# Optimization experiments

Hardware: AMD Instinct MI355X
Metric: run time of the kernel (lower is better)

The kernel has to match this reference:

```python
import jax, jax.numpy as jnp
import numpy as np

N = 8192          # num nodes
E = 262144        # num edges (avg degree 32)
D_IN = 512        # input feature dim
LAT = 128         # latent_dim


def gcn_conv(x, W, b, row, col, n):
    """PyG GCNConv: gcn_norm adds self-loops (weight 1), symmetric normalization,
    message = norm * (x @ W)[row], aggregated at col, plus bias."""
    sl = jnp.arange(n)
    r = jnp.concatenate([row, sl])
    c = jnp.concatenate([col, sl])
    deg = jax.ops.segment_sum(jnp.ones(r.shape[0], dtype=x.dtype), c, num_segments=n)
    dis = jnp.where(deg > 0, deg ** -0.5, 0.0).astype(x.dtype)
    norm = dis[r] * dis[c]                      # [E']
    h = x @ W                                   # [n, out]
    out = jax.ops.segment_sum(h[r] * norm[:, None], c, num_segments=n)
    return out + b


def setup_inputs() -> dict:
    key = jax.random.key(0)
    ks = jax.random.split(key, 12)
    x = jax.random.normal(ks[0], (N, D_IN), dtype=jnp.float32)
    edge_index = jax.random.randint(ks[1], (2, E), 0, N, dtype=jnp.int64)
    h1 = 2 * LAT
    W1 = jax.random.normal(ks[2], (D_IN, h1), dtype=jnp.float32) * (1.0 / np.sqrt(D_IN))
    b1 = jnp.zeros((h1,), dtype=jnp.float32)
    W2 = jax.random.normal(ks[3], (h1, LAT), dtype=jnp.float32) * (1.0 / np.sqrt(h1))
    b2 = jnp.zeros((LAT,), dtype=jnp.float32)
    Wmu = jax.random.normal(ks[4], (LAT, LAT), dtype=jnp.float32) * (1.0 / np.sqrt(LAT))
    bmu = jnp.zeros((LAT,), dtype=jnp.float32)
    Wlv = jax.random.normal(ks[5], (LAT, LAT), dtype=jnp.float32) * (1.0 / np.sqrt(LAT))
    blv = jnp.zeros((LAT,), dtype=jnp.float32)
    return {"x": x, "edge_index": edge_index, "W1": W1, "b1": b1, "W2": W2,
            "b2": b2, "Wmu": Wmu, "bmu": bmu, "Wlv": Wlv, "blv": blv}


def reference(x, edge_index, W1, b1, W2, b2, Wmu, bmu, Wlv, blv):
    n = x.shape[0]
    # GraphVAE.forward: add_self_loops(edge_index) once (GCNConv's gcn_norm adds them again)
    sl = jnp.arange(n)
    row = jnp.concatenate([edge_index[0], sl])
    col = jnp.concatenate([edge_index[1], sl])
    z = jax.nn.relu(gcn_conv(x, W1, b1, row, col, n))
    z = gcn_conv(z, W2, b2, row, col, n)
    mu = z @ Wmu + bmu
    logvar = z @ Wlv + blv
    # eval-mode reparameterize: z = mu (deterministic)
    adj = jax.nn.sigmoid(mu @ mu.T)   # [N, N]
    return adj, mu, logvar
```

## Files before the change

### kernel.cpp

```cpp
#include <hip/hip_runtime.h>
#include <hip/hip_bf16.h>

#define NNODES 8192
#define DIN 512
#define HD1 256
#define LATD 128
#define CAP 128

typedef __attribute__((ext_vector_type(4))) float f32x4;
typedef __attribute__((ext_vector_type(8))) short short8;

__device__ __forceinline__ float bf2f(uint u){
  union { uint i; float f; } v; v.i = u << 16; return v.f;
}
__device__ __forceinline__ ushort f2bf(float f){
  union { float f; uint i; } v; v.f = f;
  uint i = v.i;
  i += 0x7FFFu + ((i >> 16) & 1u);
  return (ushort)(i >> 16);
}


__global__ __launch_bounds__(256) void k_init(const float* __restrict__ W1,
    const float* __restrict__ W2, const float* __restrict__ Wmu,
    const float* __restrict__ Wlv, int* __restrict__ cnt,
    ushort* __restrict__ W1b, ushort* __restrict__ W2b, ushort* __restrict__ Wcb)
{
  const int stride = gridDim.x * 256;
  const int i = blockIdx.x * 256 + threadIdx.x;
  if (i < NNODES) cnt[i] = 0;
  for (int j = i; j < DIN * HD1; j += stride) W1b[j] = f2bf(W1[j]);
  for (int j = i; j < HD1 * LATD; j += stride) W2b[j] = f2bf(W2[j]);
  for (int j = i; j < LATD * 2 * LATD; j += stride){
    const int k = j >> 8, n = j & 255;
    Wcb[j] = f2bf(n < LATD ? Wmu[k * LATD + n] : Wlv[k * LATD + n - LATD]);
  }
}


__global__ __launch_bounds__(256) void k_fill_gemm1(const int* __restrict__ erow,
    const int* __restrict__ ecol, int E, int nbF,
    int* __restrict__ cursor, int* __restrict__ csr,
    const float* __restrict__ x, const ushort* __restrict__ W1b, ushort* __restrict__ h1)
{
  if ((int)blockIdx.x < nbF){
    int e = blockIdx.x * 256 + threadIdx.x;
    if (e < E){
      int r = erow[e], c = ecol[e];
      int pos = atomicAdd(&cursor[c], 1);
      if (pos < CAP) csr[(size_t)c * CAP + pos] = r;
    }
    return;
  }
  const int bx = blockIdx.x - nbF;
  const int n0 = (bx & 3) * 64, m0 = (bx >> 2) * 64;
  __shared__ ushort Al[64][40];
  __shared__ ushort Bl[64][40];
  const int t = threadIdx.x, w = t >> 6, l = t & 63, lr = l & 15, lk = l >> 4;
  const int wm = (w >> 1) * 32, wn = (w & 1) * 32;
  f32x4 acc[2][2] = {};
  for (int kt = 0; kt < DIN / 32; ++kt){
    {
      const int row = t >> 2, ch = t & 3;
      const float* ap = x + (size_t)(m0 + row) * DIN + kt * 32 + ch * 8;
      float4 v0 = *(const float4*)ap;
      float4 v1 = *(const float4*)(ap + 4);
      ushort* d = &Al[row][ch * 8];
      d[0] = f2bf(v0.x); d[1] = f2bf(v0.y); d[2] = f2bf(v0.z); d[3] = f2bf(v0.w);
      d[4] = f2bf(v1.x); d[5] = f2bf(v1.y); d[6] = f2bf(v1.z); d[7] = f2bf(v1.w);
      const int kk = t >> 3, nn = (t & 7) * 8;
      short8 bv = *(const short8*)(W1b + (size_t)(kt * 32 + kk) * HD1 + n0 + nn);
      #pragma unroll
      for (int i = 0; i < 8; ++i) Bl[nn + i][kk] = ((ushort*)&bv)[i];
    }
    __syncthreads();
    short8 a0 = *(const short8*)(&Al[wm + lr][lk * 8]);
    short8 a1 = *(const short8*)(&Al[wm + 16 + lr][lk * 8]);
    short8 b0 = *(const short8*)(&Bl[wn + lr][lk * 8]);
    short8 b1 = *(const short8*)(&Bl[wn + 16 + lr][lk * 8]);
    acc[0][0] = __builtin_amdgcn_mfma_f32_16x16x32_bf16(a0, b0, acc[0][0], 0, 0, 0);
    acc[0][1] = __builtin_amdgcn_mfma_f32_16x16x32_bf16(a0, b1, acc[0][1], 0, 0, 0);
    acc[1][0] = __builtin_amdgcn_mfma_f32_16x16x32_bf16(a1, b0, acc[1][0], 0, 0, 0);
    acc[1][1] = __builtin_amdgcn_mfma_f32_16x16x32_bf16(a1, b1, acc[1][1], 0, 0, 0);
    __syncthreads();
  }
  #pragma unroll
  for (int mi = 0; mi < 2; ++mi){
    #pragma unroll
    for (int ni = 0; ni < 2; ++ni){
      const int row = m0 + wm + mi * 16 + lk * 4;
      const int col = n0 + wn + ni * 16 + lr;
      #pragma unroll
      for (int r = 0; r < 4; ++r)
        h1[(size_t)(row + r) * HD1 + col] = f2bf(acc[mi][ni][r]);
    }
  }
}


__global__ __launch_bounds__(256) void gemm2_kernel(const ushort* __restrict__ A,
    const ushort* __restrict__ Bb, ushort* __restrict__ Cb)
{
  __shared__ ushort Al[32][40];
  __shared__ ushort Bl[64][40];
  const int t = threadIdx.x, w = t >> 6, l = t & 63, lr = l & 15, lk = l >> 4;
  const int m0 = blockIdx.y * 32, n0 = blockIdx.x * 64;
  const int wm = (w >> 1) * 16, wn = (w & 1) * 32;
  f32x4 acc[2] = {};
  for (int kt = 0; kt < HD1 / 32; ++kt){
    {
      const int row = t >> 3, ch = (t & 7) * 4;
      *(uint2*)(&Al[row][ch]) = *(const uint2*)(A + (size_t)(m0 + row) * HD1 + kt * 32 + ch);
      const int kk = t >> 3, nn = (t & 7) * 8;
      short8 bv = *(const short8*)(Bb + (size_t)(kt * 32 + kk) * LATD + n0 + nn);
      #pragma unroll
      for (int i = 0; i < 8; ++i) Bl[nn + i][kk] = ((ushort*)&bv)[i];
    }
    __syncthreads();
    short8 a = *(const short8*)(&Al[wm + lr][lk * 8]);
    short8 b0 = *(const short8*)(&Bl[wn + lr][lk * 8]);
    short8 b1 = *(const short8*)(&Bl[wn + 16 + lr][lk * 8]);
    acc[0] = __builtin_amdgcn_mfma_f32_16x16x32_bf16(a, b0, acc[0], 0, 0, 0);
    acc[1] = __builtin_amdgcn_mfma_f32_16x16x32_bf16(a, b1, acc[1], 0, 0, 0);
    __syncthreads();
  }
  #pragma unroll
  for (int ni = 0; ni < 2; ++ni){
    const int row = m0 + wm + lk * 4;
    const int col = n0 + wn + ni * 16 + lr;
    #pragma unroll
    for (int r = 0; r < 4; ++r)
      Cb[(size_t)(row + r) * LATD + col] = f2bf(acc[ni][r]);
  }
}


__global__ __launch_bounds__(256) void gemm_mulv(const ushort* __restrict__ A,
    const ushort* __restrict__ Bb, const float* __restrict__ bmu,
    const float* __restrict__ blv, float* __restrict__ mu,
    ushort* __restrict__ mu_bf, float* __restrict__ lv)
{
  __shared__ ushort Al[64][40];
  __shared__ ushort Bl[64][40];
  const int t = threadIdx.x, w = t >> 6, l = t & 63, lr = l & 15, lk = l >> 4;
  const int n0 = blockIdx.x * 64, m0 = blockIdx.y * 64;
  const bool is_mu = n0 < LATD;
  const int wm = (w >> 1) * 32, wn = (w & 1) * 32;
  f32x4 acc[2][2] = {};
  for (int kt = 0; kt < LATD / 32; ++kt){
    {
      const int row = t >> 2, ch = t & 3;
      *(short8*)(&Al[row][ch * 8]) =
        *(const short8*)(A + (size_t)(m0 + row) * LATD + kt * 32 + ch * 8);
      const int kk = t >> 3, nn = (t & 7) * 8;
      short8 bv = *(const short8*)(Bb + (size_t)(kt * 32 + kk) * (2 * LATD) + n0 + nn);
      #pragma unroll
      for (int i = 0; i < 8; ++i) Bl[nn + i][kk] = ((ushort*)&bv)[i];
    }
    __syncthreads();
    short8 a0 = *(const short8*)(&Al[wm + lr][lk * 8]);
    short8 a1 = *(const short8*)(&Al[wm + 16 + lr][lk * 8]);
    short8 b0 = *(const short8*)(&Bl[wn + lr][lk * 8]);
    short8 b1 = *(const short8*)(&Bl[wn + 16 + lr][lk * 8]);
    acc[0][0] = __builtin_amdgcn_mfma_f32_16x16x32_bf16(a0, b0, acc[0][0], 0, 0, 0);
    acc[0][1] = __builtin_amdgcn_mfma_f32_16x16x32_bf16(a0, b1, acc[0][1], 0, 0, 0);
    acc[1][0] = __builtin_amdgcn_mfma_f32_16x16x32_bf16(a1, b0, acc[1][0], 0, 0, 0);
    acc[1][1] = __builtin_amdgcn_mfma_f32_16x16x32_bf16(a1, b1, acc[1][1], 0, 0, 0);
    __syncthreads();
  }
  #pragma unroll
  for (int mi = 0; mi < 2; ++mi){
    #pragma unroll
    for (int ni = 0; ni < 2; ++ni){
      const int row = m0 + wm + mi * 16 + lk * 4;
      const int col = n0 + wn + ni * 16 + lr;
      const float bb = is_mu ? bmu[col] : blv[col - LATD];
      #pragma unroll
      for (int r = 0; r < 4; ++r){
        const float v = acc[mi][ni][r] + bb;
        if (is_mu){
          mu[(size_t)(row + r) * LATD + col] = v;
          mu_bf[(size_t)(row + r) * LATD + col] = f2bf(v);
        } else {
          lv[(size_t)(row + r) * LATD + col - LATD] = v;
        }
      }
    }
  }
}


template<int F, bool RELU>
__global__ __launch_bounds__(256) void agg_kernel(const ushort* __restrict__ h,
    const float* __restrict__ bias, const int* __restrict__ cnt,
    const int* __restrict__ csr, ushort* __restrict__ out)
{
  constexpr int LPE = F / 8;
  constexpr int EPI = 64 / LPE;
  __shared__ int2 meta[4][64];
  const int w = threadIdx.x >> 6, l = threadIdx.x & 63;
  const int v = blockIdx.x * 4 + w;
  const int deg = min(cnt[v], CAP);
  const float dv = rsqrtf((float)(deg + 2));
  const int sub = l / LPE;
  const int eb = (l % LPE) * 8;
  float acc[8] = {0.f, 0.f, 0.f, 0.f, 0.f, 0.f, 0.f, 0.f};

  const int beg = v * CAP, end = beg + deg;
  for (int base = beg; base < end; base += 64){
    const int cc = min(64, end - base);
    int idx = 0; float nr = 0.f;
    if (base + l < end){
      idx = csr[base + l];
      nr = rsqrtf((float)(min(cnt[idx], CAP) + 2)) * dv;
    }
    int2 m; m.x = idx; m.y = __float_as_int(nr);
    meta[w][l] = m;
    asm volatile("s_waitcnt lgkmcnt(0)" ::: "memory");
    const int nIt = (cc + EPI - 1) / EPI;
    for (int it = 0; it < nIt; ++it){
      int2 mm = meta[w][it * EPI + sub];
      const float nrr = __int_as_float(mm.y);
      const uint4 r = *(const uint4*)(h + (size_t)mm.x * F + eb);
      acc[0] += nrr * bf2f(r.x & 0xffff); acc[1] += nrr * bf2f(r.x >> 16);
      acc[2] += nrr * bf2f(r.y & 0xffff); acc[3] += nrr * bf2f(r.y >> 16);
      acc[4] += nrr * bf2f(r.z & 0xffff); acc[5] += nrr * bf2f(r.z >> 16);
      acc[6] += nrr * bf2f(r.w & 0xffff); acc[7] += nrr * bf2f(r.w >> 16);
    }
    asm volatile("s_waitcnt lgkmcnt(0)" ::: "memory");
  }
  #pragma unroll
  for (int off = LPE; off < 64; off <<= 1){
    #pragma unroll
    for (int j = 0; j < 8; ++j) acc[j] += __shfl_xor(acc[j], off);
  }
  if (l < LPE){
    const float ss = 2.f * dv * dv;
    const uint4 r = *(const uint4*)(h + (size_t)v * F + eb);
    acc[0] += ss * bf2f(r.x & 0xffff); acc[1] += ss * bf2f(r.x >> 16);
    acc[2] += ss * bf2f(r.y & 0xffff); acc[3] += ss * bf2f(r.y >> 16);
    acc[4] += ss * bf2f(r.z & 0xffff); acc[5] += ss * bf2f(r.z >> 16);
    acc[6] += ss * bf2f(r.w & 0xffff); acc[7] += ss * bf2f(r.w >> 16);
    float4 b0 = *(const float4*)(bias + eb);
    float4 b1 = *(const float4*)(bias + eb + 4);
    acc[0] += b0.x; acc[1] += b0.y; acc[2] += b0.z; acc[3] += b0.w;
    acc[4] += b1.x; acc[5] += b1.y; acc[6] += b1.z; acc[7] += b1.w;
    if (RELU){
      #pragma unroll
      for (int j = 0; j < 8; ++j) acc[j] = fmaxf(acc[j], 0.f);
    }
    uint4 o;
    o.x = (uint)f2bf(acc[0]) | ((uint)f2bf(acc[1]) << 16);
    o.y = (uint)f2bf(acc[2]) | ((uint)f2bf(acc[3]) << 16);
    o.z = (uint)f2bf(acc[4]) | ((uint)f2bf(acc[5]) << 16);
    o.w = (uint)f2bf(acc[6]) | ((uint)f2bf(acc[7]) << 16);
    *(uint4*)(out + (size_t)v * F + eb) = o;
  }
}


__global__ __launch_bounds__(512) void gemm5_kernel(const ushort* __restrict__ mu,
                                                    float* __restrict__ adj)
{
  __shared__ char lds[65536];
  const int t = threadIdx.x;
  const int bj = blockIdx.x, bi = blockIdx.y;
  {
    const int row = t >> 2, ch = t & 3;
    const char* srcA = (const char*)(mu + (size_t)(bi * 128 + row) * LATD);
    const char* srcB = (const char*)(mu + (size_t)(bj * 128 + row) * LATD);
    char* dA = lds + row * 256;
    char* dB = lds + 32768 + row * 256;
    #pragma unroll
    for (int i = 0; i < 4; ++i){
      const int kb = ch * 64 + i * 16;
      const int sk = kb ^ ((row & 7) << 4);
      *(short8*)(dA + sk) = *(const short8*)(srcA + kb);
      *(short8*)(dB + sk) = *(const short8*)(srcB + kb);
    }
  }
  __syncthreads();
  const int wid = t >> 6, l = t & 63, lr = l & 15, lk = l >> 4;
  const int wm = (wid >> 2) * 64, wn = (wid & 3) * 32;
  f32x4 acc[4][2] = {};
  #pragma unroll
  for (int ks = 0; ks < 4; ++ks){
    short8 a[4], b[2];
    const int kb = ks * 64 + lk * 16;
    #pragma unroll
    for (int mi = 0; mi < 4; ++mi){
      const int r = wm + mi * 16 + lr;
      a[mi] = *(const short8*)(lds + r * 256 + (kb ^ ((r & 7) << 4)));
    }
    #pragma unroll
    for (int ni = 0; ni < 2; ++ni){
      const int r = wn + ni * 16 + lr;
      b[ni] = *(const short8*)(lds + 32768 + r * 256 + (kb ^ ((r & 7) << 4)));
    }
    #pragma unroll
    for (int mi = 0; mi < 4; ++mi)
      #pragma unroll
      for (int ni = 0; ni < 2; ++ni)
        acc[mi][ni] = __builtin_amdgcn_mfma_f32_16x16x32_bf16(a[mi], b[ni], acc[mi][ni], 0, 0, 0);
  }
  float* orow = adj + (size_t)(bi * 128 + wm + lk * 4) * NNODES + bj * 128 + wn + lr;
  #pragma unroll
  for (int mi = 0; mi < 4; ++mi){
    #pragma unroll
    for (int ni = 0; ni < 2; ++ni){
      #pragma unroll
      for (int r = 0; r < 4; ++r){
        const float x = acc[mi][ni][r];
        orow[(size_t)(mi * 16 + r) * NNODES + ni * 16] = 1.f / (1.f + __expf(-x));
      }
    }
  }
}


extern "C" void kernel_launch(void* const* d_in, const int* in_sizes, int n_in,
                              void* d_out, int out_size, void* d_ws, size_t ws_size,
                              hipStream_t stream)
{
  const float* x    = (const float*)d_in[0];
  const int*   ei   = (const int*)d_in[1];
  const float* W1   = (const float*)d_in[2];
  const float* b1   = (const float*)d_in[3];
  const float* W2   = (const float*)d_in[4];
  const float* b2   = (const float*)d_in[5];
  const float* Wmu  = (const float*)d_in[6];
  const float* bmu  = (const float*)d_in[7];
  const float* Wlv  = (const float*)d_in[8];
  const float* blv  = (const float*)d_in[9];
  const int E = in_sizes[1] / 2;
  const int* erow = ei;
  const int* ecol = ei + E;

  char* ws = (char*)d_ws;
  int*    cnt   = (int*)(ws);
  ushort* W1b   = (ushort*)(ws + 65536);
  ushort* W2b   = (ushort*)(ws + 327680);
  ushort* Wcb   = (ushort*)(ws + 393216);
  int*    csr   = (int*)(ws + 1048576);
  ushort* h1    = (ushort*)(ws + 8388608);
  ushort* z1    = (ushort*)(ws + 12582912);
  ushort* h2    = (ushort*)(ws + 16777216);
  ushort* z2    = (ushort*)(ws + 18874368);
  ushort* mu_bf = (ushort*)(ws + 20971520);

  float* adj = (float*)d_out;
  float* mu  = adj + (size_t)NNODES * NNODES;
  float* lv  = mu + (size_t)NNODES * LATD;

  const int nbF = (E + 255) / 256;

  k_init<<<128, 256, 0, stream>>>(W1, W2, Wmu, Wlv, cnt, W1b, W2b, Wcb);
  k_fill_gemm1<<<nbF + 4 * (NNODES / 64), 256, 0, stream>>>(
      erow, ecol, E, nbF, cnt, csr, x, W1b, h1);
  agg_kernel<HD1, true><<<NNODES / 4, 256, 0, stream>>>(h1, b1, cnt, csr, z1);
  gemm2_kernel<<<dim3(LATD / 64, NNODES / 32), 256, 0, stream>>>(z1, W2b, h2);
  agg_kernel<LATD, false><<<NNODES / 4, 256, 0, stream>>>(h2, b2, cnt, csr, z2);
  gemm_mulv<<<dim3(2 * LATD / 64, NNODES / 64), 256, 0, stream>>>(
      z2, Wcb, bmu, blv, mu, mu_bf, lv);
  gemm5_kernel<<<dim3(NNODES / 128, NNODES / 128), 512, 0, stream>>>(mu_bf, adj);
}
```

Before: 129.2 us.

## Reorder second GCN layer as aggregate-then-GEMM and fuse with mu/logvar GEMM

The second GCN layer now aggregates z1 (width 256) first and then multiplies by W2, using linearity (A·(z1·W2) = (A·z1)·W2). The W2 GEMM and the mu/logvar GEMM are fused into one kernel that keeps z2 in LDS. GEMM1 and the fused kernel load operands straight from global memory into registers, using weights pre-transposed to a K-contiguous layout, so the LDS staging and barriers are gone. The cost is a second aggregation pass at width 256 instead of 128, which doubles that gather traffic, plus a one-time strided weight transpose.

Result: slower. 168.3 us (+30.3%).

```diff
diff --git a/kernel.cpp b/kernel.cpp
--- a/kernel.cpp
+++ b/kernel.cpp
@@ -19,21 +19,49 @@
   i += 0x7FFFu + ((i >> 16) & 1u);
   return (ushort)(i >> 16);
 }
+__device__ __forceinline__ short8 pack8(float4 v0, float4 v1){
+  short8 s;
+  s[0] = (short)f2bf(v0.x); s[1] = (short)f2bf(v0.y);
+  s[2] = (short)f2bf(v0.z); s[3] = (short)f2bf(v0.w);
+  s[4] = (short)f2bf(v1.x); s[5] = (short)f2bf(v1.y);
+  s[6] = (short)f2bf(v1.z); s[7] = (short)f2bf(v1.w);
+  return s;
+}
 
 
 __global__ __launch_bounds__(256) void k_init(const float* __restrict__ W1,
     const float* __restrict__ W2, const float* __restrict__ Wmu,
     const float* __restrict__ Wlv, int* __restrict__ cnt,
-    ushort* __restrict__ W1b, ushort* __restrict__ W2b, ushort* __restrict__ Wcb)
+    ushort* __restrict__ W1t, ushort* __restrict__ W2t, ushort* __restrict__ Wct)
 {
   const int stride = gridDim.x * 256;
-  const int i = blockIdx.x * 256 + threadIdx.x;
-  if (i < NNODES) cnt[i] = 0;
-  for (int j = i; j < DIN * HD1; j += stride) W1b[j] = f2bf(W1[j]);
-  for (int j = i; j < HD1 * LATD; j += stride) W2b[j] = f2bf(W2[j]);
-  for (int j = i; j < LATD * 2 * LATD; j += stride){
-    const int k = j >> 8, n = j & 255;
-    Wcb[j] = f2bf(n < LATD ? Wmu[k * LATD + n] : Wlv[k * LATD + n - LATD]);
+  const int gid = blockIdx.x * 256 + threadIdx.x;
+  if (gid < NNODES) cnt[gid] = 0;
+  for (int j = gid; j < HD1 * (DIN / 8); j += stride){
+    const int kc = j >> 8, n = j & 255;
+    short8 s;
+    #pragma unroll
+    for (int jj = 0; jj < 8; ++jj) s[jj] = (short)f2bf(W1[(size_t)(kc * 8 + jj) * HD1 + n]);
+    *(short8*)(W1t + (size_t)n * DIN + kc * 8) = s;
+  }
+  for (int j = gid; j < LATD * (HD1 / 8); j += stride){
+    const int kc = j >> 7, n = j & 127;
+    short8 s;
+    #pragma unroll
+    for (int jj = 0; jj < 8; ++jj) s[jj] = (short)f2bf(W2[(size_t)(kc * 8 + jj) * LATD + n]);
+    *(short8*)(W2t + (size_t)n * HD1 + kc * 8) = s;
+  }
+  for (int j = gid; j < 2 * LATD * (LATD / 8); j += stride){
+    const int kc = j >> 8, n = j & 255;
+    short8 s;
+    if (n < LATD){
+      #pragma unroll
+      for (int jj = 0; jj < 8; ++jj) s[jj] = (short)f2bf(Wmu[(size_t)(kc * 8 + jj) * LATD + n]);
+    } else {
+      #pragma unroll
+      for (int jj = 0; jj < 8; ++jj) s[jj] = (short)f2bf(Wlv[(size_t)(kc * 8 + jj) * LATD + n - LATD]);
+    }
+    *(short8*)(Wct + (size_t)n * LATD + kc * 8) = s;
   }
 }
 
@@ -41,7 +69,7 @@
 __global__ __launch_bounds__(256) void k_fill_gemm1(const int* __restrict__ erow,
     const int* __restrict__ ecol, int E, int nbF,
     int* __restrict__ cursor, int* __restrict__ csr,
-    const float* __restrict__ x, const ushort* __restrict__ W1b, ushort* __restrict__ h1)
+    const float* __restrict__ x, const ushort* __restrict__ W1t, ushort* __restrict__ h1)
 {
   if ((int)blockIdx.x < nbF){
     int e = blockIdx.x * 256 + threadIdx.x;
@@ -54,35 +82,24 @@
   }
   const int bx = blockIdx.x - nbF;
   const int n0 = (bx & 3) * 64, m0 = (bx >> 2) * 64;
-  __shared__ ushort Al[64][40];
-  __shared__ ushort Bl[64][40];
   const int t = threadIdx.x, w = t >> 6, l = t & 63, lr = l & 15, lk = l >> 4;
   const int wm = (w >> 1) * 32, wn = (w & 1) * 32;
   f32x4 acc[2][2] = {};
+  const float* ar0 = x + (size_t)(m0 + wm + lr) * DIN;
+  const float* ar1 = x + (size_t)(m0 + wm + 16 + lr) * DIN;
+  const ushort* br0 = W1t + (size_t)(n0 + wn + lr) * DIN;
+  const ushort* br1 = W1t + (size_t)(n0 + wn + 16 + lr) * DIN;
+  #pragma unroll 4
   for (int kt = 0; kt < DIN / 32; ++kt){
-    {
-      const int row = t >> 2, ch = t & 3;
-      const float* ap = x + (size_t)(m0 + row) * DIN + kt * 32 + ch * 8;
-      float4 v0 = *(const float4*)ap;
-      float4 v1 = *(const float4*)(ap + 4);
-      ushort* d = &Al[row][ch * 8];
-      d[0] = f2bf(v0.x); d[1] = f2bf(v0.y); d[2] = f2bf(v0.z); d[3] = f2bf(v0.w);
-      d[4] = f2bf(v1.x); d[5] = f2bf(v1.y); d[6] = f2bf(v1.z); d[7] = f2bf(v1.w);
-      const int kk = t >> 3, nn = (t & 7) * 8;
-      short8 bv = *(const short8*)(W1b + (size_t)(kt * 32 + kk) * HD1 + n0 + nn);
-      #pragma unroll
-      for (int i = 0; i < 8; ++i) Bl[nn + i][kk] = ((ushort*)&bv)[i];
-    }
-    __syncthreads();
-    short8 a0 = *(const short8*)(&Al[wm + lr][lk * 8]);
-    short8 a1 = *(const short8*)(&Al[wm + 16 + lr][lk * 8]);
-    short8 b0 = *(const short8*)(&Bl[wn + lr][lk * 8]);
-    short8 b1 = *(const short8*)(&Bl[wn + 16 + lr][lk * 8]);
+    const int ko = kt * 32 + lk * 8;
+    short8 a0 = pack8(*(const float4*)(ar0 + ko), *(const float4*)(ar0 + ko + 4));
+    short8 a1 = pack8(*(const float4*)(ar1 + ko), *(const float4*)(ar1 + ko + 4));
+    short8 b0 = *(const short8*)(br0 + ko);
+    short8 b1 = *(const short8*)(br1 + ko);
     acc[0][0] = __builtin_amdgcn_mfma_f32_16x16x32_bf16(a0, b0, acc[0][0], 0, 0, 0);
     acc[0][1] = __builtin_amdgcn_mfma_f32_16x16x32_bf16(a0, b1, acc[0][1], 0, 0, 0);
     acc[1][0] = __builtin_amdgcn_mfma_f32_16x16x32_bf16(a1, b0, acc[1][0], 0, 0, 0);
     acc[1][1] = __builtin_amdgcn_mfma_f32_16x16x32_bf16(a1, b1, acc[1][1], 0, 0, 0);
-    __syncthreads();
   }
   #pragma unroll
   for (int mi = 0; mi < 2; ++mi){
@@ -98,103 +115,12 @@
 }
 
 
-__global__ __launch_bounds__(256) void gemm2_kernel(const ushort* __restrict__ A,
-    const ushort* __restrict__ Bb, ushort* __restrict__ Cb)
-{
-  __shared__ ushort Al[32][40];
-  __shared__ ushort Bl[64][40];
-  const int t = threadIdx.x, w = t >> 6, l = t & 63, lr = l & 15, lk = l >> 4;
-  const int m0 = blockIdx.y * 32, n0 = blockIdx.x * 64;
-  const int wm = (w >> 1) * 16, wn = (w & 1) * 32;
-  f32x4 acc[2] = {};
-  for (int kt = 0; kt < HD1 / 32; ++kt){
-    {
-      const int row = t >> 3, ch = (t & 7) * 4;
-      *(uint2*)(&Al[row][ch]) = *(const uint2*)(A + (size_t)(m0 + row) * HD1 + kt * 32 + ch);
-      const int kk = t >> 3, nn = (t & 7) * 8;
-      short8 bv = *(const short8*)(Bb + (size_t)(kt * 32 + kk) * LATD + n0 + nn);
-      #pragma unroll
-      for (int i = 0; i < 8; ++i) Bl[nn + i][kk] = ((ushort*)&bv)[i];
-    }
-    __syncthreads();
-    short8 a = *(const short8*)(&Al[wm + lr][lk * 8]);
-    short8 b0 = *(const short8*)(&Bl[wn + lr][lk * 8]);
-    short8 b1 = *(const short8*)(&Bl[wn + 16 + lr][lk * 8]);
-    acc[0] = __builtin_amdgcn_mfma_f32_16x16x32_bf16(a, b0, acc[0], 0, 0, 0);
-    acc[1] = __builtin_amdgcn_mfma_f32_16x16x32_bf16(a, b1, acc[1], 0, 0, 0);
-    __syncthreads();
-  }
-  #pragma unroll
-  for (int ni = 0; ni < 2; ++ni){
-    const int row = m0 + wm + lk * 4;
-    const int col = n0 + wn + ni * 16 + lr;
-    #pragma unroll
-    for (int r = 0; r < 4; ++r)
-      Cb[(size_t)(row + r) * LATD + col] = f2bf(acc[ni][r]);
-  }
-}
-
-
-__global__ __launch_bounds__(256) void gemm_mulv(const ushort* __restrict__ A,
-    const ushort* __restrict__ Bb, const float* __restrict__ bmu,
-    const float* __restrict__ blv, float* __restrict__ mu,
-    ushort* __restrict__ mu_bf, float* __restrict__ lv)
-{
-  __shared__ ushort Al[64][40];
-  __shared__ ushort Bl[64][40];
-  const int t = threadIdx.x, w = t >> 6, l = t & 63, lr = l & 15, lk = l >> 4;
-  const int n0 = blockIdx.x * 64, m0 = blockIdx.y * 64;
-  const bool is_mu = n0 < LATD;
-  const int wm = (w >> 1) * 32, wn = (w & 1) * 32;
-  f32x4 acc[2][2] = {};
-  for (int kt = 0; kt < LATD / 32; ++kt){
-    {
-      const int row = t >> 2, ch = t & 3;
-      *(short8*)(&Al[row][ch * 8]) =
-        *(const short8*)(A + (size_t)(m0 + row) * LATD + kt * 32 + ch * 8);
-      const int kk = t >> 3, nn = (t & 7) * 8;
-      short8 bv = *(const short8*)(Bb + (size_t)(kt * 32 + kk) * (2 * LATD) + n0 + nn);
-      #pragma unroll
-      for (int i = 0; i < 8; ++i) Bl[nn + i][kk] = ((ushort*)&bv)[i];
-    }
-    __syncthreads();
-    short8 a0 = *(const short8*)(&Al[wm + lr][lk * 8]);
-    short8 a1 = *(const short8*)(&Al[wm + 16 + lr][lk * 8]);
-    short8 b0 = *(const short8*)(&Bl[wn + lr][lk * 8]);
-    short8 b1 = *(const short8*)(&Bl[wn + 16 + lr][lk * 8]);
-    acc[0][0] = __builtin_amdgcn_mfma_f32_16x16x32_bf16(a0, b0, acc[0][0], 0, 0, 0);
-    acc[0][1] = __builtin_amdgcn_mfma_f32_16x16x32_bf16(a0, b1, acc[0][1], 0, 0, 0);
-    acc[1][0] = __builtin_amdgcn_mfma_f32_16x16x32_bf16(a1, b0, acc[1][0], 0, 0, 0);
-    acc[1][1] = __builtin_amdgcn_mfma_f32_16x16x32_bf16(a1, b1, acc[1][1], 0, 0, 0);
-    __syncthreads();
-  }
-  #pragma unroll
-  for (int mi = 0; mi < 2; ++mi){
-    #pragma unroll
-    for (int ni = 0; ni < 2; ++ni){
-      const int row = m0 + wm + mi * 16 + lk * 4;
-      const int col = n0 + wn + ni * 16 + lr;
-      const float bb = is_mu ? bmu[col] : blv[col - LATD];
-      #pragma unroll
-      for (int r = 0; r < 4; ++r){
-        const float v = acc[mi][ni][r] + bb;
-        if (is_mu){
-          mu[(size_t)(row + r) * LATD + col] = v;
-          mu_bf[(size_t)(row + r) * LATD + col] = f2bf(v);
-        } else {
-          lv[(size_t)(row + r) * LATD + col - LATD] = v;
-        }
-      }
-    }
-  }
-}
-
-
-template<int F, bool RELU>
+template<bool RELU, bool HASB>
 __global__ __launch_bounds__(256) void agg_kernel(const ushort* __restrict__ h,
     const float* __restrict__ bias, const int* __restrict__ cnt,
     const int* __restrict__ csr, ushort* __restrict__ out)
 {
+  constexpr int F = 256;
   constexpr int LPE = F / 8;
   constexpr int EPI = 64 / LPE;
   __shared__ int2 meta[4][64];
@@ -241,10 +167,12 @@
     acc[2] += ss * bf2f(r.y & 0xffff); acc[3] += ss * bf2f(r.y >> 16);
     acc[4] += ss * bf2f(r.z & 0xffff); acc[5] += ss * bf2f(r.z >> 16);
     acc[6] += ss * bf2f(r.w & 0xffff); acc[7] += ss * bf2f(r.w >> 16);
-    float4 b0 = *(const float4*)(bias + eb);
-    float4 b1 = *(const float4*)(bias + eb + 4);
-    acc[0] += b0.x; acc[1] += b0.y; acc[2] += b0.z; acc[3] += b0.w;
-    acc[4] += b1.x; acc[5] += b1.y; acc[6] += b1.z; acc[7] += b1.w;
+    if (HASB){
+      float4 b0 = *(const float4*)(bias + eb);
+      float4 b1 = *(const float4*)(bias + eb + 4);
+      acc[0] += b0.x; acc[1] += b0.y; acc[2] += b0.z; acc[3] += b0.w;
+      acc[4] += b1.x; acc[5] += b1.y; acc[6] += b1.z; acc[7] += b1.w;
+    }
     if (RELU){
       #pragma unroll
       for (int j = 0; j < 8; ++j) acc[j] = fmaxf(acc[j], 0.f);
@@ -255,6 +183,82 @@
     o.z = (uint)f2bf(acc[4]) | ((uint)f2bf(acc[5]) << 16);
     o.w = (uint)f2bf(acc[6]) | ((uint)f2bf(acc[7]) << 16);
     *(uint4*)(out + (size_t)v * F + eb) = o;
+  }
+}
+
+
+__global__ __launch_bounds__(256) void k_z2mulv(const ushort* __restrict__ y,
+    const ushort* __restrict__ W2t, const ushort* __restrict__ Wct,
+    const float* __restrict__ b2, const float* __restrict__ bmu,
+    const float* __restrict__ blv, float* __restrict__ mu,
+    ushort* __restrict__ mu_bf, float* __restrict__ lv)
+{
+  __shared__ ushort z2t[64][136];
+  const int t = threadIdx.x, w = t >> 6, l = t & 63, lr = l & 15, lk = l >> 4;
+  const int m0 = blockIdx.x * 64;
+  {
+    const int wm = w * 16;
+    f32x4 acc[8] = {};
+    const ushort* ar = y + (size_t)(m0 + wm + lr) * HD1;
+    #pragma unroll
+    for (int kt = 0; kt < HD1 / 32; ++kt){
+      const int ko = kt * 32 + lk * 8;
+      short8 a = *(const short8*)(ar + ko);
+      #pragma unroll
+      for (int ni = 0; ni < 8; ++ni){
+        short8 b = *(const short8*)(W2t + (size_t)(ni * 16 + lr) * HD1 + ko);
+        acc[ni] = __builtin_amdgcn_mfma_f32_16x16x32_bf16(a, b, acc[ni], 0, 0, 0);
+      }
+    }
+    #pragma unroll
+    for (int ni = 0; ni < 8; ++ni){
+      const int col = ni * 16 + lr;
+      const float bb = b2[col];
+      #pragma unroll
+      for (int r = 0; r < 4; ++r)
+        z2t[wm + lk * 4 + r][col] = f2bf(acc[ni][r] + bb);
+    }
+  }
+  __syncthreads();
+  {
+    const int wm2 = (w >> 1) * 32, wn2 = (w & 1) * 128;
+    const bool is_mu = (wn2 == 0);
+    f32x4 acc[2][8] = {};
+    #pragma unroll
+    for (int kt = 0; kt < LATD / 32; ++kt){
+      const int ko = kt * 32 + lk * 8;
+      short8 a0 = *(const short8*)(&z2t[wm2 + lr][ko]);
+      short8 a1 = *(const short8*)(&z2t[wm2 + 16 + lr][ko]);
+      #pragma unroll
+      for (int ni = 0; ni < 8; ++ni){
+        short8 b = *(const short8*)(Wct + (size_t)(wn2 + ni * 16 + lr) * LATD + ko);
+        acc[0][ni] = __builtin_amdgcn_mfma_f32_16x16x32_bf16(a0, b, acc[0][ni], 0, 0, 0);
+        acc[1][ni] = __builtin_amdgcn_mfma_f32_16x16x32_bf16(a1, b, acc[1][ni], 0, 0, 0);
+      }
+    }
+    #pragma unroll
+    for (int mi = 0; mi < 2; ++mi){
+      #pragma unroll
+      for (int ni = 0; ni < 8; ++ni){
+        const int row = m0 + wm2 + mi * 16 + lk * 4;
+        const int gcol = wn2 + ni * 16 + lr;
+        if (is_mu){
+          const float bb = bmu[gcol];
+          #pragma unroll
+          for (int r = 0; r < 4; ++r){
+            const float v = acc[mi][ni][r] + bb;
+            mu[(size_t)(row + r) * LATD + gcol] = v;
+            mu_bf[(size_t)(row + r) * LATD + gcol] = f2bf(v);
+          }
+        } else {
+          const int c = gcol - LATD;
+          const float bb = blv[c];
+          #pragma unroll
+          for (int r = 0; r < 4; ++r)
+            lv[(size_t)(row + r) * LATD + c] = acc[mi][ni][r] + bb;
+        }
+      }
+    }
   }
 }
 
@@ -338,14 +342,13 @@
 
   char* ws = (char*)d_ws;
   int*    cnt   = (int*)(ws);
-  ushort* W1b   = (ushort*)(ws + 65536);
-  ushort* W2b   = (ushort*)(ws + 327680);
-  ushort* Wcb   = (ushort*)(ws + 393216);
+  ushort* W1t   = (ushort*)(ws + 65536);
+  ushort* W2t   = (ushort*)(ws + 327680);
+  ushort* Wct   = (ushort*)(ws + 393216);
   int*    csr   = (int*)(ws + 1048576);
   ushort* h1    = (ushort*)(ws + 8388608);
   ushort* z1    = (ushort*)(ws + 12582912);
-  ushort* h2    = (ushort*)(ws + 16777216);
-  ushort* z2    = (ushort*)(ws + 18874368);
+  ushort* y     = (ushort*)(ws + 16777216);
   ushort* mu_bf = (ushort*)(ws + 20971520);
 
   float* adj = (float*)d_out;
@@ -354,13 +357,11 @@
 
   const int nbF = (E + 255) / 256;
 
-  k_init<<<128, 256, 0, stream>>>(W1, W2, Wmu, Wlv, cnt, W1b, W2b, Wcb);
+  k_init<<<128, 256, 0, stream>>>(W1, W2, Wmu, Wlv, cnt, W1t, W2t, Wct);
   k_fill_gemm1<<<nbF + 4 * (NNODES / 64), 256, 0, stream>>>(
-      erow, ecol, E, nbF, cnt, csr, x, W1b, h1);
-  agg_kernel<HD1, true><<<NNODES / 4, 256, 0, stream>>>(h1, b1, cnt, csr, z1);
-  gemm2_kernel<<<dim3(LATD / 64, NNODES / 32), 256, 0, stream>>>(z1, W2b, h2);
-  agg_kernel<LATD, false><<<NNODES / 4, 256, 0, stream>>>(h2, b2, cnt, csr, z2);
-  gemm_mulv<<<dim3(2 * LATD / 64, NNODES / 64), 256, 0, stream>>>(
-      z2, Wcb, bmu, blv, mu, mu_bf, lv);
+      erow, ecol, E, nbF, cnt, csr, x, W1t, h1);
+  agg_kernel<true, true><<<NNODES / 4, 256, 0, stream>>>(h1, b1, cnt, csr, z1);
+  agg_kernel<false, false><<<NNODES / 4, 256, 0, stream>>>(z1, nullptr, cnt, csr, y);
+  k_z2mulv<<<NNODES / 64, 256, 0, stream>>>(y, W2t, Wct, b2, bmu, blv, mu, mu_bf, lv);
   gemm5_kernel<<<dim3(NNODES / 128, NNODES / 128), 512, 0, stream>>>(mu_bf, adj);
 }
```
